# Performance work log

Hardware: AMD Instinct MI355X
Metric: run time of the kernel (lower is better)

The kernel has to match this reference:

```python
import jax, jax.numpy as jnp
import numpy as np

N_CLASSES = 24
ATT_CLASS = 5  # attention_class init kwarg
NS_GRAPHS, NQ_GRAPHS, NODES_PER_G = 48, 24, 4
BN_EPS = 1e-5
COS_EPS = 1e-6


def _conv3(x, w):
    return jax.lax.conv_general_dilated(x, w, (1, 1), 'SAME',
                                        dimension_numbers=('NCHW', 'OIHW', 'NCHW'))


def _maxpool2(x):
    return jax.lax.reduce_window(x, -jnp.inf, jax.lax.max, (1, 1, 2, 2), (1, 1, 2, 2), 'VALID')


def _bn_train(x, g, b):
    # BatchNorm2d in training mode: batch statistics over (N,H,W), biased variance
    m = x.mean(axis=(0, 2, 3), keepdims=True)
    v = x.var(axis=(0, 2, 3), keepdims=True)
    return (x - m) * jax.lax.rsqrt(v + BN_EPS) * g.reshape(1, -1, 1, 1) + b.reshape(1, -1, 1, 1)


def _block(x, w, g, b):
    return _maxpool2(jax.nn.relu(_bn_train(_conv3(x, w), g, b)))


def _cnn(x, w1, g1, b1, w2, g2, b2, w_rest, g_rest, b_rest):
    x = _block(x, w1, g1, b1)
    x = _block(x, w2, g2, b2)
    for i in range(4):  # fixed small layer loop
        x = _block(x, w_rest[i], g_rest[i], b_rest[i])
    return x.reshape(x.shape[0], -1)  # [N, 64*2*2 = 256]


def _seg_mean(v, idx, n):
    s = jax.ops.segment_sum(v, idx, num_segments=n)
    c = jax.ops.segment_sum(jnp.ones(idx.shape, v.dtype), idx, num_segments=n)
    c = jnp.maximum(c, 1.0)
    return s / (c if v.ndim == 1 else c[:, None])


def _edge_cos_per_node(x, edge_index, n_nodes):
    src, dst = edge_index[0], edge_index[1]
    xj, xi = x[src], x[dst]  # gather per edge
    dot = jnp.sum(xj * xi, axis=-1)
    denom = jnp.maximum(jnp.linalg.norm(xj, axis=-1) * jnp.linalg.norm(xi, axis=-1), COS_EPS)
    cos = dot / denom
    return _seg_mean(cos, dst, n_nodes)  # scatter-mean onto target nodes


def _make_edges(key, n_graphs, epg):
    k1, k2 = jax.random.split(key)
    base = jnp.repeat(jnp.arange(n_graphs, dtype=jnp.int32) * NODES_PER_G, epg)
    src = base + jax.random.randint(k1, base.shape, 0, NODES_PER_G, dtype=jnp.int32)
    dst = base + jax.random.randint(k2, base.shape, 0, NODES_PER_G, dtype=jnp.int32)
    return jnp.stack([src, dst])


def setup_inputs() -> dict:
    key = jax.random.key(0)
    ks = jax.random.split(key, 12)
    ns, nq = NS_GRAPHS * NODES_PER_G, NQ_GRAPHS * NODES_PER_G
    support_x = jax.random.normal(ks[0], (ns, 3, 128, 128), jnp.float32)
    query_x = jax.random.normal(ks[1], (nq, 3, 128, 128), jnp.float32)
    support_edge_index = _make_edges(ks[2], NS_GRAPHS, 16)  # [2,768]
    query_edge_index = _make_edges(ks[3], NQ_GRAPHS, 16)    # [2,384]
    support_batch = jnp.repeat(jnp.arange(NS_GRAPHS, dtype=jnp.int32), NODES_PER_G)
    query_batch = jnp.repeat(jnp.arange(NQ_GRAPHS, dtype=jnp.int32), NODES_PER_G)
    support_y = jnp.tile(jnp.arange(N_CLASSES, dtype=jnp.int32), NS_GRAPHS // N_CLASSES)
    query_y = jnp.arange(N_CLASSES, dtype=jnp.int32)
    def he(k, shp):
        fan_in = shp[1] * shp[2] * shp[3] if len(shp) == 4 else shp[2] * shp[3] * shp[4]
        return jax.random.normal(k, shp, jnp.float32) * np.float32(np.sqrt(2.0 / fan_in))
    w1 = he(ks[4], (32, 3, 3, 3))
    w2 = he(ks[5], (64, 32, 3, 3))
    w_rest = he(ks[6], (4, 64, 64, 3, 3))
    g1 = 1.0 + 0.1 * jax.random.normal(ks[7], (32,), jnp.float32)
    b1 = 0.1 * jax.random.normal(ks[8], (32,), jnp.float32)
    g2 = 1.0 + 0.1 * jax.random.normal(ks[9], (64,), jnp.float32)
    b2 = 0.1 * jax.random.normal(ks[10], (64,), jnp.float32)
    g_rest = 1.0 + 0.1 * jax.random.normal(ks[11], (4, 64), jnp.float32)
    b_rest = 0.1 * jax.random.normal(jax.random.fold_in(key, 99), (4, 64), jnp.float32)
    return {'support_x': support_x, 'query_x': query_x,
            'support_edge_index': support_edge_index, 'query_edge_index': query_edge_index,
            'support_batch': support_batch, 'query_batch': query_batch,
            'support_y': support_y, 'query_y': query_y,
            'w1': w1, 'g1': g1, 'b1': b1, 'w2': w2, 'g2': g2, 'b2': b2,
            'w_rest': w_rest, 'g_rest': g_rest, 'b_rest': b_rest}


def reference(support_x, query_x, w1, g1, b1, w2, g2, b2, w_rest, g_rest, b_rest,
              support_edge_index, query_edge_index, support_batch, query_batch,
              support_y, query_y):
    ns, nq = support_x.shape[0], query_x.shape[0]
    # CNN node features (MEConv.mlp), per torch-geometric call semantics: separate BN stats per call
    s_x = _cnn(support_x, w1, g1, b1, w2, g2, b2, w_rest, g_rest, b_rest)  # [Ns, 256]
    q_x = _cnn(query_x, w1, g1, b1, w2, g2, b2, w_rest, g_rest, b_rest)    # [Nq, 256]
    # message: cosine similarity per edge, aggregate: scatter-mean to target nodes
    s_cos_node = _edge_cos_per_node(s_x, support_edge_index, ns)  # [Ns]
    # per-graph pooled features (scatter mean over batch); note the original discards
    # the aggregated neighbor-mean output and uses the raw node features here
    s_cat = _seg_mean(s_x, support_batch, NS_GRAPHS)  # [Gs, 256]
    p_cat = _seg_mean(q_x, query_batch, NQ_GRAPHS)    # [Gq, 256]
    # RBF distance between each query prototype and every support graph (vectorized loop)
    pd1 = jnp.exp(-jnp.sum((p_cat[:, None, :] - s_cat[None, :, :]) ** 2, axis=-1))  # [Gq, Gs]
    # cosine alignment loss
    s_cos_graph = _seg_mean(s_cos_node, support_batch, NS_GRAPHS)
    cos_loss = jnp.sum((s_cos_graph - 1.0) ** 2)
    # class-wise scatter-mean of distances over support labels
    csum = jax.ops.segment_sum(pd1.T, support_y, num_segments=N_CLASSES)  # [24, Gq]
    ccnt = jnp.maximum(jax.ops.segment_sum(jnp.ones((NS_GRAPHS,), pd1.dtype), support_y,
                                           num_segments=N_CLASSES), 1.0)
    output = (csum / ccnt[:, None]).T  # [Gq, 24]
    # cross-entropy with one-hot soft targets, split by the static attention mask
    label = jax.nn.one_hot(query_y, N_CLASSES, dtype=output.dtype)
    ce_rows = -jnp.sum(label * jax.nn.log_softmax(output, axis=-1), axis=-1)  # [Gq]
    atten_loss = ce_rows[ATT_CLASS]                       # mask selects the single attention class row
    rest_loss = (jnp.sum(ce_rows) - atten_loss) / (N_CLASSES - 1)
    loss = atten_loss + rest_loss + cos_loss
    acc = jnp.sum((jnp.argmax(output, axis=1) == query_y).astype(jnp.float32))
    return loss, acc, cos_loss, atten_loss, rest_loss
```

## Files before the change

kernel.cpp:

```cpp
#include <hip/hip_runtime.h>
#include <hip/hip_bf16.h>
#include <cstdint>
#include <cstddef>


template<int IC, int OC, int H, int TS, int OCG, bool PREBN>
__global__ __launch_bounds__(TS*TS/4)
void conv_stats(const float* __restrict__ inA, const float* __restrict__ inB,
                int nSplit, const float* __restrict__ W,
                const float* __restrict__ pscl, const float* __restrict__ pshf,
                double* __restrict__ stats, float* __restrict__ maxout,
                int nSupport)
{
  constexpr int TH = TS/2;
  constexpr int NT = TH*TH;
  constexpr int NW = (NT+63)/64;
  constexpr int TILES = H/TS;
  constexpr int SH = TILES*TILES;
  constexpr int OCGN = OC/OCG;
  constexpr int SZ = (TS+2)*(TS+2);

  const int tid = threadIdx.x;

  const int w     = blockIdx.x % (8*OCGN);
  const int chunk = blockIdx.x / (8*OCGN);
  const int ocg   = w >> 3;
  const int slot  = chunk*8 + (w & 7);
  const int n     = slot / SH;
  const int t     = slot % SH;
  const int ty0 = (t / TILES) * TS;
  const int tx0 = (t % TILES) * TS;

  const float* in = (n < nSplit) ? inA + (size_t)n*IC*H*H
                                 : inB + (size_t)(n - nSplit)*IC*H*H;
  const float* Wb = W + (size_t)(ocg*OCG)*IC*9;
  const int g = (n < nSupport) ? 0 : 1;

  __shared__ float sIn[2][SZ];
  __shared__ float sSum[NW][OCG], sSsq[NW][OCG];

  float acc[4][OCG];
  #pragma unroll
  for (int i = 0; i < 4; ++i)
    #pragma unroll
    for (int o = 0; o < OCG; ++o) acc[i][o] = 0.f;

  const int tx = tid % TH, ty = tid / TH;
  const int iy = 2*ty, ix = 2*tx;

  for (int ic = 0; ic < IC; ++ic) {
    float* sBuf = sIn[ic & 1];
    const float* ip = in + (size_t)ic*H*H;
    float ps = 0.f, pt = 0.f;
    if constexpr (PREBN) { ps = pscl[g*IC + ic]; pt = pshf[g*IC + ic]; }
    for (int i = tid; i < SZ; i += NT) {
      int r = i/(TS+2), c = i%(TS+2);
      int gy = ty0 + r - 1, gx = tx0 + c - 1;
      float v = 0.f;
      if (gy >= 0 && gy < H && gx >= 0 && gx < H) {
        v = ip[gy*H + gx];
        if constexpr (PREBN)
          v = fmaxf(fmaf(v, ps, pt), 0.f);
      }
      sBuf[i] = v;
    }
    __syncthreads();

    float xr[4][4];
    #pragma unroll
    for (int r = 0; r < 4; ++r)
      #pragma unroll
      for (int c = 0; c < 4; ++c)
        xr[r][c] = sBuf[(iy+r)*(TS+2) + ix + c];

    #pragma unroll
    for (int oc = 0; oc < OCG; ++oc) {
      const float* wp = Wb + (size_t)oc*IC*9 + ic*9;
      float w9[9];
      #pragma unroll
      for (int k = 0; k < 9; ++k) w9[k] = wp[k];
      #pragma unroll
      for (int kh = 0; kh < 3; ++kh) {
        #pragma unroll
        for (int kw = 0; kw < 3; ++kw) {
          const float wv = w9[kh*3 + kw];
          acc[0][oc] = fmaf(xr[kh  ][kw  ], wv, acc[0][oc]);
          acc[1][oc] = fmaf(xr[kh  ][kw+1], wv, acc[1][oc]);
          acc[2][oc] = fmaf(xr[kh+1][kw  ], wv, acc[2][oc]);
          acc[3][oc] = fmaf(xr[kh+1][kw+1], wv, acc[3][oc]);
        }
      }
    }
  }

  {
    const int py = ty0/2 + ty, px = tx0/2 + tx;
    #pragma unroll
    for (int oc = 0; oc < OCG; ++oc) {
      const int ocGl = ocg*OCG + oc;
      float mx = fmaxf(fmaxf(acc[0][oc], acc[1][oc]),
                       fmaxf(acc[2][oc], acc[3][oc]));
      maxout[(((size_t)n*OC + ocGl)*(H/2) + py)*(H/2) + px] = mx;
    }
  }

  const int lane = tid & 63, wid = tid >> 6;
  #pragma unroll
  for (int oc = 0; oc < OCG; ++oc) {
    float ls = acc[0][oc] + acc[1][oc] + acc[2][oc] + acc[3][oc];
    float lq = acc[0][oc]*acc[0][oc] + acc[1][oc]*acc[1][oc]
             + acc[2][oc]*acc[2][oc] + acc[3][oc]*acc[3][oc];
    #pragma unroll
    for (int off = 32; off > 0; off >>= 1) {
      ls += __shfl_down(ls, off);
      lq += __shfl_down(lq, off);
    }
    if (lane == 0) { sSum[wid][oc] = ls; sSsq[wid][oc] = lq; }
  }
  __syncthreads();
  if (tid < OCG) {
    float S = 0.f, Q = 0.f;
    #pragma unroll
    for (int w2 = 0; w2 < NW; ++w2) { S += sSum[w2][tid]; Q += sSsq[w2][tid]; }
    const int ocGl = ocg*OCG + tid;
    atomicAdd(&stats[(g*OC + ocGl)*2 + 0], (double)S);
    atomicAdd(&stats[(g*OC + ocGl)*2 + 1], (double)Q);
  }
}

template<int H, bool APPLY, bool PREBN>
__global__ __launch_bounds__(256)
void conv_small(const float* __restrict__ in, const float* __restrict__ W,
                const float* __restrict__ pscl, const float* __restrict__ pshf,
                const float* __restrict__ scale, const float* __restrict__ shift,
                double* __restrict__ stats, float* __restrict__ out, int nSupport)
{
  constexpr int HW = H*H;
  constexpr int NACC = (H == 8) ? 16 : 4;
  constexpr int SC = (H == 4) ? 64*16 : 1;
  const int tid = threadIdx.x;
  const int n  = blockIdx.x;
  const int oc = tid & 63;
  const int q  = tid >> 6;
  const int g = (n < nSupport) ? 0 : 1;

  __shared__ float sX[64*HW];
  __shared__ float sS[256];
  __shared__ float sQ[256];
  __shared__ float sC[SC];

  for (int i = tid; i < 64*HW; i += 256) {
    float v = in[(size_t)n*64*HW + i];
    if constexpr (PREBN) {
      int ic = i / HW;
      v = fmaxf(fmaf(v, pscl[g*64 + ic], pshf[g*64 + ic]), 0.f);
    }
    sX[i] = v;
  }
  __syncthreads();

  float acc[NACC];
  #pragma unroll
  for (int i = 0; i < NACC; ++i) acc[i] = 0.f;

  const int ry = (H == 8) ? 4*(q >> 1) : 0;
  const int rx = (H == 8) ? 4*(q & 1)  : 0;

  for (int ic = 0; ic < 64; ++ic) {
    const float* wp = W + ((size_t)oc*64 + ic)*9;
    float w[9];
    #pragma unroll
    for (int k = 0; k < 9; ++k) w[k] = wp[k];
    if (H == 8) {
      float rin[6][6];
      #pragma unroll
      for (int r = 0; r < 6; ++r) {
        int y = ry + r - 1;
        #pragma unroll
        for (int c = 0; c < 6; ++c) {
          int x = rx + c - 1;
          rin[r][c] = (y >= 0 && y < H && x >= 0 && x < H) ? sX[ic*HW + y*H + x] : 0.f;
        }
      }
      #pragma unroll
      for (int kh = 0; kh < 3; ++kh)
        #pragma unroll
        for (int kw = 0; kw < 3; ++kw) {
          float wv = w[kh*3+kw];
          #pragma unroll
          for (int py = 0; py < 4; ++py)
            #pragma unroll
            for (int px = 0; px < 4; ++px)
              acc[py*4+px] = fmaf(wv, rin[py+kh][px+kw], acc[py*4+px]);
        }
    } else {
      float rin[3][6];
      #pragma unroll
      for (int r = 0; r < 3; ++r) {
        int y = q + r - 1;
        #pragma unroll
        for (int c = 0; c < 6; ++c) {
          int x = c - 1;
          rin[r][c] = (y >= 0 && y < H && x >= 0 && x < H) ? sX[ic*HW + y*H + x] : 0.f;
        }
      }
      #pragma unroll
      for (int kh = 0; kh < 3; ++kh)
        #pragma unroll
        for (int kw = 0; kw < 3; ++kw) {
          float wv = w[kh*3+kw];
          #pragma unroll
          for (int px = 0; px < 4; ++px)
            acc[px] = fmaf(wv, rin[kh][px+kw], acc[px]);
        }
    }
  }

  if constexpr (APPLY) {
    float s = scale[g*64 + oc];
    float t = shift[g*64 + oc];
    if (H == 8) {
      const int py0 = ry/2, px0 = rx/2;
      #pragma unroll
      for (int pj = 0; pj < 2; ++pj)
        #pragma unroll
        for (int pi = 0; pi < 2; ++pi) {
          float v0 = fmaxf(fmaf(acc[(2*pj  )*4 + 2*pi  ], s, t), 0.f);
          float v1 = fmaxf(fmaf(acc[(2*pj  )*4 + 2*pi+1], s, t), 0.f);
          float v2 = fmaxf(fmaf(acc[(2*pj+1)*4 + 2*pi  ], s, t), 0.f);
          float v3 = fmaxf(fmaf(acc[(2*pj+1)*4 + 2*pi+1], s, t), 0.f);
          out[(((size_t)n*64 + oc)*4 + (py0+pj))*4 + (px0+pi)] =
              fmaxf(fmaxf(v0, v1), fmaxf(v2, v3));
        }
    } else {
      #pragma unroll
      for (int px = 0; px < 4; ++px)
        sC[oc*16 + q*4 + px] = fmaxf(fmaf(acc[px], s, t), 0.f);
      __syncthreads();
      int oc2 = tid & 63, pj = (tid >> 6) & 1, pi = (tid >> 7) & 1;
      float m = fmaxf(
          fmaxf(sC[oc2*16 + (2*pj  )*4 + 2*pi], sC[oc2*16 + (2*pj  )*4 + 2*pi+1]),
          fmaxf(sC[oc2*16 + (2*pj+1)*4 + 2*pi], sC[oc2*16 + (2*pj+1)*4 + 2*pi+1]));
      out[(((size_t)n*64 + oc2)*2 + pj)*2 + pi] = m;
    }
  } else {
    float ls = 0.f, lq = 0.f;
    #pragma unroll
    for (int i = 0; i < NACC; ++i) { ls += acc[i]; lq += acc[i]*acc[i]; }
    sS[tid] = ls; sQ[tid] = lq;
    __syncthreads();
    if (tid < 64) {
      float S = sS[tid] + sS[tid+64] + sS[tid+128] + sS[tid+192];
      float Q = sQ[tid] + sQ[tid+64] + sQ[tid+128] + sQ[tid+192];
      atomicAdd(&stats[(g*64 + tid)*2 + 0], (double)S);
      atomicAdd(&stats[(g*64 + tid)*2 + 1], (double)Q);
    }
  }
}

__global__ void bn_finalize(const double* __restrict__ stats,
                            const float* __restrict__ gamma, const float* __restrict__ beta,
                            float* __restrict__ scale, float* __restrict__ shift,
                            int OC, double cnt0, double cnt1)
{
  int i = threadIdx.x;
  if (i < 2*OC) {
    int oc = i % OC;
    double cnt = (i < OC) ? cnt0 : cnt1;
    double mean = stats[i*2 + 0] / cnt;
    double var  = stats[i*2 + 1] / cnt - mean*mean;
    double inv  = 1.0 / sqrt(var + 1e-5);
    double g = (double)gamma[oc];
    double b = (double)beta[oc];
    scale[i] = (float)(g * inv);
    shift[i] = (float)(b - mean * g * inv);
  }
}

__global__ void graph_means(const float* __restrict__ feat,
                            float* __restrict__ s_cat, float* __restrict__ p_cat)
{
  int g = blockIdx.x, d = threadIdx.x;
  if (g < 48) {
    float v = 0.f;
    for (int i = 0; i < 4; ++i) v += feat[(size_t)(4*g + i)*256 + d];
    s_cat[g*256 + d] = v * 0.25f;
  } else {
    int q = g - 48;
    float v = 0.f;
    for (int i = 0; i < 4; ++i) v += feat[(size_t)(192 + 4*q + i)*256 + d];
    p_cat[q*256 + d] = v * 0.25f;
  }
}

__global__ void edge_cos(const float* __restrict__ feat, const int* __restrict__ ei,
                         float* __restrict__ nsum, float* __restrict__ ncnt, int nEdges)
{
  int e = blockIdx.x, lane = threadIdx.x;
  int src = ei[e], dst = ei[nEdges + e];
  float dot = 0.f, nj = 0.f, ni = 0.f;
  for (int j = lane; j < 256; j += 64) {
    float a = feat[(size_t)src*256 + j];
    float b = feat[(size_t)dst*256 + j];
    dot += a*b; nj += a*a; ni += b*b;
  }
  for (int off = 32; off > 0; off >>= 1) {
    dot += __shfl_down(dot, off);
    nj  += __shfl_down(nj,  off);
    ni  += __shfl_down(ni,  off);
  }
  if (lane == 0) {
    float denom = fmaxf(sqrtf(nj)*sqrtf(ni), 1e-6f);
    atomicAdd(&nsum[dst], dot/denom);
    atomicAdd(&ncnt[dst], 1.f);
  }
}

__global__ void cos_loss_k(const float* __restrict__ nsum, const float* __restrict__ ncnt,
                           float* __restrict__ cosloss)
{
  int g = threadIdx.x;
  float v = 0.f;
  if (g < 48) {
    float gm = 0.f;
    for (int i = 0; i < 4; ++i) {
      int nd = 4*g + i;
      gm += nsum[nd] / fmaxf(ncnt[nd], 1.f);
    }
    gm *= 0.25f;
    v = (gm - 1.f)*(gm - 1.f);
  }
  for (int off = 32; off > 0; off >>= 1) v += __shfl_down(v, off);
  if (g == 0) cosloss[0] = v;
}

__global__ void pd_out(const float* __restrict__ s_cat, const float* __restrict__ p_cat,
                       const int* __restrict__ support_y, const int* __restrict__ query_y,
                       float* __restrict__ ce, float* __restrict__ correct)
{
  const int q = blockIdx.x;
  const int tid = threadIdx.x, lane = tid & 63, wid = tid >> 6;
  __shared__ float sP[48];
  __shared__ float sOut[24];
  float pv[4];
  #pragma unroll
  for (int j = 0; j < 4; ++j) pv[j] = p_cat[(size_t)q*256 + lane + 64*j];
  for (int s = wid*12; s < wid*12 + 12; ++s) {
    float d2 = 0.f;
    #pragma unroll
    for (int j = 0; j < 4; ++j) {
      float diff = pv[j] - s_cat[(size_t)s*256 + lane + 64*j];
      d2 += diff*diff;
    }
    for (int off = 32; off > 0; off >>= 1) d2 += __shfl_down(d2, off);
    if (lane == 0) sP[s] = expf(-d2);
  }
  __syncthreads();
  if (tid < 24) {
    int c = tid; float sum = 0.f; int cnt = 0;
    for (int s = 0; s < 48; ++s)
      if (support_y[s] == c) { sum += sP[s]; ++cnt; }
    sOut[c] = sum / fmaxf((float)cnt, 1.f);
  }
  __syncthreads();
  if (tid == 0) {
    float m = sOut[0]; int am = 0;
    for (int c = 1; c < 24; ++c) if (sOut[c] > m) { m = sOut[c]; am = c; }
    float lse = 0.f;
    for (int c = 0; c < 24; ++c) lse += expf(sOut[c] - m);
    lse = m + logf(lse);
    int y = query_y[q];
    ce[q] = lse - sOut[y];
    correct[q] = (am == y) ? 1.f : 0.f;
  }
}

__global__ void final_k(const float* __restrict__ ce, const float* __restrict__ correct,
                        const float* __restrict__ cosloss, float* __restrict__ out)
{
  if (threadIdx.x == 0) {
    float s = 0.f, a = 0.f;
    for (int qq = 0; qq < 24; ++qq) { s += ce[qq]; a += correct[qq]; }
    float atten = ce[5];
    float rest  = (s - atten) / 23.f;
    float cl = cosloss[0];
    out[0] = atten + rest + cl;
    out[1] = a;
    out[2] = cl;
    out[3] = atten;
    out[4] = rest;
  }
}

extern "C" void kernel_launch(void* const* d_in, const int* in_sizes, int n_in,
                              void* d_out, int out_size, void* d_ws, size_t ws_size,
                              hipStream_t stream)
{
  const float* support_x = (const float*)d_in[0];
  const float* query_x   = (const float*)d_in[1];
  const int*   s_ei      = (const int*)d_in[2];
  const int*   s_y       = (const int*)d_in[6];
  const int*   q_y       = (const int*)d_in[7];
  const float* w1 = (const float*)d_in[8];
  const float* g1 = (const float*)d_in[9];
  const float* b1 = (const float*)d_in[10];
  const float* w2 = (const float*)d_in[11];
  const float* g2 = (const float*)d_in[12];
  const float* b2 = (const float*)d_in[13];
  const float* wr = (const float*)d_in[14];
  const float* gr = (const float*)d_in[15];
  const float* br = (const float*)d_in[16];
  (void)in_sizes; (void)n_in; (void)out_size;

  char* ws = (char*)d_ws;
  size_t off = 0;
  auto alloc = [&](size_t bytes) -> char* {
    char* p = ws + off;
    off = (off + bytes + 255) & ~(size_t)255;
    return p;
  };
  float*  actA  = (float*)alloc((size_t)288*32*64*64*4);
  float*  actB  = (float*)alloc((size_t)288*64*32*32*4);
  double* stats = (double*)alloc(6*256*8);
  float*  scl   = (float*)alloc(6*128*4);
  float*  shf   = (float*)alloc(6*128*4);
  float*  s_cat = (float*)alloc(48*256*4);
  float*  p_cat = (float*)alloc(24*256*4);
  float*  nsum  = (float*)alloc(192*4);
  float*  ncnt  = (float*)alloc(192*4);
  float*  cosl  = (float*)alloc(256);
  float*  ce    = (float*)alloc(24*4);
  float*  corr  = (float*)alloc(24*4);
  if (off > ws_size) return;

  const int NS = 192;
  const int BIG = 1 << 30;

  float* mx3   = actA;
  float* mx4   = actA + (size_t)288*64*16*16;
  float* l5out = mx4  + (size_t)288*64*8*8;
  float* feat  = l5out + (size_t)288*64*4*4;

  hipMemsetAsync(stats, 0, 6*256*8, stream);
  hipMemsetAsync(nsum, 0, 192*4, stream);
  hipMemsetAsync(ncnt, 0, 192*4, stream);

  conv_stats<3,32,128,32,16,false><<<9216,256,0,stream>>>(
      support_x, query_x, 192, w1, nullptr, nullptr, stats, actA, NS);
  bn_finalize<<<1,128,0,stream>>>(stats, g1, b1, scl, shf, 32,
      192.0*128*128, 96.0*128*128);

  conv_stats<32,64,64,32,16,true><<<4608,256,0,stream>>>(
      actA, actA, BIG, w2, scl, shf, stats+256, actB, NS);
  bn_finalize<<<1,128,0,stream>>>(stats+256, g2, b2, scl+128, shf+128, 64,
      192.0*64*64, 96.0*64*64);

  conv_stats<64,64,32,32,16,true><<<1152,256,0,stream>>>(
      actB, actB, BIG, wr + 0*36864, scl+128, shf+128, stats+512, mx3, NS);
  bn_finalize<<<1,128,0,stream>>>(stats+512, gr + 0*64, br + 0*64,
      scl+256, shf+256, 64, 192.0*32*32, 96.0*32*32);

  conv_stats<64,64,16,16,4,true><<<4608,64,0,stream>>>(
      mx3, mx3, BIG, wr + 1*36864, scl+256, shf+256, stats+768, mx4, NS);
  bn_finalize<<<1,128,0,stream>>>(stats+768, gr + 1*64, br + 1*64,
      scl+384, shf+384, 64, 192.0*16*16, 96.0*16*16);

  conv_small<8,false,true><<<288,256,0,stream>>>(
      mx4, wr + 2*36864, scl+384, shf+384, nullptr, nullptr, stats+1024, nullptr, NS);
  bn_finalize<<<1,128,0,stream>>>(stats+1024, gr + 2*64, br + 2*64,
      scl+512, shf+512, 64, 192.0*8*8, 96.0*8*8);
  conv_small<8,true,true><<<288,256,0,stream>>>(
      mx4, wr + 2*36864, scl+384, shf+384, scl+512, shf+512, nullptr, l5out, NS);

  conv_small<4,false,false><<<288,256,0,stream>>>(
      l5out, wr + 3*36864, nullptr, nullptr, nullptr, nullptr, stats+1280, nullptr, NS);
  bn_finalize<<<1,128,0,stream>>>(stats+1280, gr + 3*64, br + 3*64,
      scl+640, shf+640, 64, 192.0*4*4, 96.0*4*4);
  conv_small<4,true,false><<<288,256,0,stream>>>(
      l5out, wr + 3*36864, nullptr, nullptr, scl+640, shf+640, nullptr, feat, NS);

  graph_means<<<72,256,0,stream>>>(feat, s_cat, p_cat);
  edge_cos<<<768,64,0,stream>>>(feat, s_ei, nsum, ncnt, 768);
  cos_loss_k<<<1,64,0,stream>>>(nsum, ncnt, cosl);
  pd_out<<<24,256,0,stream>>>(s_cat, p_cat, s_y, q_y, ce, corr);
  final_k<<<1,64,0,stream>>>(ce, corr, cosl, (float*)d_out);
}
```

Measured before the change: 1.558 ms.

## Fold BN finalize into consumers and drop recompute passes in small convs

```diff
diff --git a/kernel.cpp b/kernel.cpp
--- a/kernel.cpp
+++ b/kernel.cpp
@@ -8,7 +8,8 @@
 __global__ __launch_bounds__(TS*TS/4)
 void conv_stats(const float* __restrict__ inA, const float* __restrict__ inB,
                 int nSplit, const float* __restrict__ W,
-                const float* __restrict__ pscl, const float* __restrict__ pshf,
+                const double* __restrict__ pstats, const float* __restrict__ pgam,
+                const float* __restrict__ pbet, double pcnt0, double pcnt1,
                 double* __restrict__ stats, float* __restrict__ maxout,
                 int nSupport)
 {
@@ -38,6 +39,21 @@
 
   __shared__ float sIn[2][SZ];
   __shared__ float sSum[NW][OCG], sSsq[NW][OCG];
+  __shared__ float sScl[PREBN ? IC : 1], sShf[PREBN ? IC : 1];
+
+  if constexpr (PREBN) {
+    for (int i = tid; i < IC; i += NT) {
+      double cnt  = (g == 0) ? pcnt0 : pcnt1;
+      double mean = pstats[((size_t)g*IC + i)*2 + 0] / cnt;
+      double var  = pstats[((size_t)g*IC + i)*2 + 1] / cnt - mean*mean;
+      double inv  = 1.0 / sqrt(var + 1e-5);
+      double ga = (double)pgam[i];
+      double be = (double)pbet[i];
+      sScl[i] = (float)(ga * inv);
+      sShf[i] = (float)(be - mean * ga * inv);
+    }
+    __syncthreads();
+  }
 
   float acc[4][OCG];
   #pragma unroll
@@ -52,7 +68,7 @@
     float* sBuf = sIn[ic & 1];
     const float* ip = in + (size_t)ic*H*H;
     float ps = 0.f, pt = 0.f;
-    if constexpr (PREBN) { ps = pscl[g*IC + ic]; pt = pshf[g*IC + ic]; }
+    if constexpr (PREBN) { ps = sScl[ic]; pt = sShf[ic]; }
     for (int i = tid; i < SZ; i += NT) {
       int r = i/(TS+2), c = i%(TS+2);
       int gy = ty0 + r - 1, gx = tx0 + c - 1;
@@ -128,11 +144,11 @@
   }
 }
 
-template<int H, bool APPLY, bool PREBN>
+template<int H>
 __global__ __launch_bounds__(256)
 void conv_small(const float* __restrict__ in, const float* __restrict__ W,
-                const float* __restrict__ pscl, const float* __restrict__ pshf,
-                const float* __restrict__ scale, const float* __restrict__ shift,
+                const double* __restrict__ pstats, const float* __restrict__ pgam,
+                const float* __restrict__ pbet, double pcnt0, double pcnt1,
                 double* __restrict__ stats, float* __restrict__ out, int nSupport)
 {
   constexpr int HW = H*H;
@@ -148,14 +164,23 @@
   __shared__ float sS[256];
   __shared__ float sQ[256];
   __shared__ float sC[SC];
+  __shared__ float sScl[64], sShf[64];
+
+  if (tid < 64) {
+    double cnt  = (g == 0) ? pcnt0 : pcnt1;
+    double mean = pstats[((size_t)g*64 + tid)*2 + 0] / cnt;
+    double var  = pstats[((size_t)g*64 + tid)*2 + 1] / cnt - mean*mean;
+    double inv  = 1.0 / sqrt(var + 1e-5);
+    double ga = (double)pgam[tid];
+    double be = (double)pbet[tid];
+    sScl[tid] = (float)(ga * inv);
+    sShf[tid] = (float)(be - mean * ga * inv);
+  }
+  __syncthreads();
 
   for (int i = tid; i < 64*HW; i += 256) {
-    float v = in[(size_t)n*64*HW + i];
-    if constexpr (PREBN) {
-      int ic = i / HW;
-      v = fmaxf(fmaf(v, pscl[g*64 + ic], pshf[g*64 + ic]), 0.f);
-    }
-    sX[i] = v;
+    int ic = i / HW;
+    sX[i] = fmaxf(fmaf(in[(size_t)n*64*HW + i], sScl[ic], sShf[ic]), 0.f);
   }
   __syncthreads();
 
@@ -216,34 +241,7 @@
     }
   }
 
-  if constexpr (APPLY) {
-    float s = scale[g*64 + oc];
-    float t = shift[g*64 + oc];
-    if (H == 8) {
-      const int py0 = ry/2, px0 = rx/2;
-      #pragma unroll
-      for (int pj = 0; pj < 2; ++pj)
-        #pragma unroll
-        for (int pi = 0; pi < 2; ++pi) {
-          float v0 = fmaxf(fmaf(acc[(2*pj  )*4 + 2*pi  ], s, t), 0.f);
-          float v1 = fmaxf(fmaf(acc[(2*pj  )*4 + 2*pi+1], s, t), 0.f);
-          float v2 = fmaxf(fmaf(acc[(2*pj+1)*4 + 2*pi  ], s, t), 0.f);
-          float v3 = fmaxf(fmaf(acc[(2*pj+1)*4 + 2*pi+1], s, t), 0.f);
-          out[(((size_t)n*64 + oc)*4 + (py0+pj))*4 + (px0+pi)] =
-              fmaxf(fmaxf(v0, v1), fmaxf(v2, v3));
-        }
-    } else {
-      #pragma unroll
-      for (int px = 0; px < 4; ++px)
-        sC[oc*16 + q*4 + px] = fmaxf(fmaf(acc[px], s, t), 0.f);
-      __syncthreads();
-      int oc2 = tid & 63, pj = (tid >> 6) & 1, pi = (tid >> 7) & 1;
-      float m = fmaxf(
-          fmaxf(sC[oc2*16 + (2*pj  )*4 + 2*pi], sC[oc2*16 + (2*pj  )*4 + 2*pi+1]),
-          fmaxf(sC[oc2*16 + (2*pj+1)*4 + 2*pi], sC[oc2*16 + (2*pj+1)*4 + 2*pi+1]));
-      out[(((size_t)n*64 + oc2)*2 + pj)*2 + pi] = m;
-    }
-  } else {
+  {
     float ls = 0.f, lq = 0.f;
     #pragma unroll
     for (int i = 0; i < NACC; ++i) { ls += acc[i]; lq += acc[i]*acc[i]; }
@@ -256,52 +254,90 @@
       atomicAdd(&stats[(g*64 + tid)*2 + 1], (double)Q);
     }
   }
-}
-
-__global__ void bn_finalize(const double* __restrict__ stats,
-                            const float* __restrict__ gamma, const float* __restrict__ beta,
-                            float* __restrict__ scale, float* __restrict__ shift,
-                            int OC, double cnt0, double cnt1)
-{
-  int i = threadIdx.x;
-  if (i < 2*OC) {
-    int oc = i % OC;
-    double cnt = (i < OC) ? cnt0 : cnt1;
-    double mean = stats[i*2 + 0] / cnt;
-    double var  = stats[i*2 + 1] / cnt - mean*mean;
+  if (H == 8) {
+    const int py0 = ry/2, px0 = rx/2;
+    #pragma unroll
+    for (int pj = 0; pj < 2; ++pj)
+      #pragma unroll
+      for (int pi = 0; pi < 2; ++pi) {
+        float mx = fmaxf(
+            fmaxf(acc[(2*pj  )*4 + 2*pi], acc[(2*pj  )*4 + 2*pi+1]),
+            fmaxf(acc[(2*pj+1)*4 + 2*pi], acc[(2*pj+1)*4 + 2*pi+1]));
+        out[(((size_t)n*64 + oc)*4 + (py0+pj))*4 + (px0+pi)] = mx;
+      }
+  } else {
+    __syncthreads();
+    #pragma unroll
+    for (int px = 0; px < 4; ++px)
+      sC[oc*16 + q*4 + px] = acc[px];
+    __syncthreads();
+    int oc2 = tid & 63, pj = (tid >> 6) & 1, pi = (tid >> 7) & 1;
+    float m = fmaxf(
+        fmaxf(sC[oc2*16 + (2*pj  )*4 + 2*pi], sC[oc2*16 + (2*pj  )*4 + 2*pi+1]),
+        fmaxf(sC[oc2*16 + (2*pj+1)*4 + 2*pi], sC[oc2*16 + (2*pj+1)*4 + 2*pi+1]));
+    out[(((size_t)n*64 + oc2)*2 + pj)*2 + pi] = m;
+  }
+}
+
+__global__ void graph_means(const float* __restrict__ raw,
+                            const double* __restrict__ st,
+                            const float* __restrict__ gam, const float* __restrict__ bet,
+                            float* __restrict__ s_cat, float* __restrict__ p_cat)
+{
+  int gb = blockIdx.x, d = threadIdx.x;
+  const int gg = (gb < 48) ? 0 : 1;
+  __shared__ float sScl[64], sShf[64];
+  if (d < 64) {
+    double cnt  = (gg == 0) ? 192.0*4*4 : 96.0*4*4;
+    double mean = st[((size_t)gg*64 + d)*2 + 0] / cnt;
+    double var  = st[((size_t)gg*64 + d)*2 + 1] / cnt - mean*mean;
     double inv  = 1.0 / sqrt(var + 1e-5);
-    double g = (double)gamma[oc];
-    double b = (double)beta[oc];
-    scale[i] = (float)(g * inv);
-    shift[i] = (float)(b - mean * g * inv);
-  }
-}
-
-__global__ void graph_means(const float* __restrict__ feat,
-                            float* __restrict__ s_cat, float* __restrict__ p_cat)
-{
-  int g = blockIdx.x, d = threadIdx.x;
-  if (g < 48) {
+    double ga = (double)gam[d];
+    double be = (double)bet[d];
+    sScl[d] = (float)(ga * inv);
+    sShf[d] = (float)(be - mean * ga * inv);
+  }
+  __syncthreads();
+  const float s = sScl[d >> 2], t = sShf[d >> 2];
+  if (gb < 48) {
     float v = 0.f;
-    for (int i = 0; i < 4; ++i) v += feat[(size_t)(4*g + i)*256 + d];
-    s_cat[g*256 + d] = v * 0.25f;
+    for (int i = 0; i < 4; ++i)
+      v += fmaxf(fmaf(raw[(size_t)(4*gb + i)*256 + d], s, t), 0.f);
+    s_cat[gb*256 + d] = v * 0.25f;
   } else {
-    int q = g - 48;
+    int qg = gb - 48;
     float v = 0.f;
-    for (int i = 0; i < 4; ++i) v += feat[(size_t)(192 + 4*q + i)*256 + d];
-    p_cat[q*256 + d] = v * 0.25f;
-  }
-}
-
-__global__ void edge_cos(const float* __restrict__ feat, const int* __restrict__ ei,
+    for (int i = 0; i < 4; ++i)
+      v += fmaxf(fmaf(raw[(size_t)(192 + 4*qg + i)*256 + d], s, t), 0.f);
+    p_cat[qg*256 + d] = v * 0.25f;
+  }
+}
+
+__global__ void edge_cos(const float* __restrict__ raw,
+                         const double* __restrict__ st,
+                         const float* __restrict__ gam, const float* __restrict__ bet,
+                         const int* __restrict__ ei,
                          float* __restrict__ nsum, float* __restrict__ ncnt, int nEdges)
 {
   int e = blockIdx.x, lane = threadIdx.x;
+  __shared__ float sScl[64], sShf[64];
+  {
+    double cnt  = 192.0*4*4;
+    double mean = st[(size_t)lane*2 + 0] / cnt;
+    double var  = st[(size_t)lane*2 + 1] / cnt - mean*mean;
+    double inv  = 1.0 / sqrt(var + 1e-5);
+    double ga = (double)gam[lane];
+    double be = (double)bet[lane];
+    sScl[lane] = (float)(ga * inv);
+    sShf[lane] = (float)(be - mean * ga * inv);
+  }
+  __syncthreads();
   int src = ei[e], dst = ei[nEdges + e];
   float dot = 0.f, nj = 0.f, ni = 0.f;
   for (int j = lane; j < 256; j += 64) {
-    float a = feat[(size_t)src*256 + j];
-    float b = feat[(size_t)dst*256 + j];
+    float s = sScl[j >> 2], t = sShf[j >> 2];
+    float a = fmaxf(fmaf(raw[(size_t)src*256 + j], s, t), 0.f);
+    float b = fmaxf(fmaf(raw[(size_t)dst*256 + j], s, t), 0.f);
     dot += a*b; nj += a*a; ni += b*b;
   }
   for (int off = 32; off > 0; off >>= 1) {
@@ -422,8 +458,6 @@
   float*  actA  = (float*)alloc((size_t)288*32*64*64*4);
   float*  actB  = (float*)alloc((size_t)288*64*32*32*4);
   double* stats = (double*)alloc(6*256*8);
-  float*  scl   = (float*)alloc(6*128*4);
-  float*  shf   = (float*)alloc(6*128*4);
   float*  s_cat = (float*)alloc(48*256*4);
   float*  p_cat = (float*)alloc(24*256*4);
   float*  nsum  = (float*)alloc(192*4);
@@ -438,49 +472,41 @@
 
   float* mx3   = actA;
   float* mx4   = actA + (size_t)288*64*16*16;
-  float* l5out = mx4  + (size_t)288*64*8*8;
-  float* feat  = l5out + (size_t)288*64*4*4;
+  float* rawm5 = mx4  + (size_t)288*64*8*8;
+  float* rawm6 = rawm5 + (size_t)288*64*4*4;
 
   hipMemsetAsync(stats, 0, 6*256*8, stream);
   hipMemsetAsync(nsum, 0, 192*4, stream);
   hipMemsetAsync(ncnt, 0, 192*4, stream);
 
   conv_stats<3,32,128,32,16,false><<<9216,256,0,stream>>>(
-      support_x, query_x, 192, w1, nullptr, nullptr, stats, actA, NS);
-  bn_finalize<<<1,128,0,stream>>>(stats, g1, b1, scl, shf, 32,
-      192.0*128*128, 96.0*128*128);
+      support_x, query_x, 192, w1, nullptr, nullptr, nullptr, 0.0, 0.0,
+      stats, actA, NS);
 
   conv_stats<32,64,64,32,16,true><<<4608,256,0,stream>>>(
-      actA, actA, BIG, w2, scl, shf, stats+256, actB, NS);
-  bn_finalize<<<1,128,0,stream>>>(stats+256, g2, b2, scl+128, shf+128, 64,
-      192.0*64*64, 96.0*64*64);
+      actA, actA, BIG, w2, stats, g1, b1, 192.0*128*128, 96.0*128*128,
+      stats+256, actB, NS);
 
   conv_stats<64,64,32,32,16,true><<<1152,256,0,stream>>>(
-      actB, actB, BIG, wr + 0*36864, scl+128, shf+128, stats+512, mx3, NS);
-  bn_finalize<<<1,128,0,stream>>>(stats+512, gr + 0*64, br + 0*64,
-      scl+256, shf+256, 64, 192.0*32*32, 96.0*32*32);
+      actB, actB, BIG, wr + 0*36864, stats+256, g2, b2, 192.0*64*64, 96.0*64*64,
+      stats+512, mx3, NS);
 
   conv_stats<64,64,16,16,4,true><<<4608,64,0,stream>>>(
-      mx3, mx3, BIG, wr + 1*36864, scl+256, shf+256, stats+768, mx4, NS);
-  bn_finalize<<<1,128,0,stream>>>(stats+768, gr + 1*64, br + 1*64,
-      scl+384, shf+384, 64, 192.0*16*16, 96.0*16*16);
-
-  conv_small<8,false,true><<<288,256,0,stream>>>(
-      mx4, wr + 2*36864, scl+384, shf+384, nullptr, nullptr, stats+1024, nullptr, NS);
-  bn_finalize<<<1,128,0,stream>>>(stats+1024, gr + 2*64, br + 2*64,
-      scl+512, shf+512, 64, 192.0*8*8, 96.0*8*8);
-  conv_small<8,true,true><<<288,256,0,stream>>>(
-      mx4, wr + 2*36864, scl+384, shf+384, scl+512, shf+512, nullptr, l5out, NS);
-
-  conv_small<4,false,false><<<288,256,0,stream>>>(
-      l5out, wr + 3*36864, nullptr, nullptr, nullptr, nullptr, stats+1280, nullptr, NS);
-  bn_finalize<<<1,128,0,stream>>>(stats+1280, gr + 3*64, br + 3*64,
-      scl+640, shf+640, 64, 192.0*4*4, 96.0*4*4);
-  conv_small<4,true,false><<<288,256,0,stream>>>(
-      l5out, wr + 3*36864, nullptr, nullptr, scl+640, shf+640, nullptr, feat, NS);
-
-  graph_means<<<72,256,0,stream>>>(feat, s_cat, p_cat);
-  edge_cos<<<768,64,0,stream>>>(feat, s_ei, nsum, ncnt, 768);
+      mx3, mx3, BIG, wr + 1*36864, stats+512, gr + 0*64, br + 0*64,
+      192.0*32*32, 96.0*32*32, stats+768, mx4, NS);
+
+  conv_small<8><<<288,256,0,stream>>>(
+      mx4, wr + 2*36864, stats+768, gr + 1*64, br + 1*64,
+      192.0*16*16, 96.0*16*16, stats+1024, rawm5, NS);
+
+  conv_small<4><<<288,256,0,stream>>>(
+      rawm5, wr + 3*36864, stats+1024, gr + 2*64, br + 2*64,
+      192.0*8*8, 96.0*8*8, stats+1280, rawm6, NS);
+
+  graph_means<<<72,256,0,stream>>>(rawm6, stats+1280, gr + 3*64, br + 3*64,
+                                   s_cat, p_cat);
+  edge_cos<<<768,64,0,stream>>>(rawm6, stats+1280, gr + 3*64, br + 3*64,
+                                s_ei, nsum, ncnt, 768);
   cos_loss_k<<<1,64,0,stream>>>(nsum, ncnt, cosl);
   pd_out<<<24,256,0,stream>>>(s_cat, p_cat, s_y, q_y, ce, corr);
   final_k<<<1,64,0,stream>>>(ce, corr, cosl, (float*)d_out);
```

After: 1.459 ms. -6.4%, faster.
